# Kernel optimization log

Hardware: AMD Instinct MI355X
Metric: run time of the kernel (lower is better)

The kernel has to match this reference:

```python
import jax, jax.numpy as jnp
import numpy as np

B, T, D_IN, H, D_OUT = 4096, 512, 8, 50, 1

def setup_inputs() -> dict:
    key = jax.random.key(0)
    ks = jax.random.split(key, 7)
    s_ih = 1.0 / np.sqrt(H)
    return {
        "x": jax.random.normal(ks[0], (B, T, D_IN), dtype=jnp.float32),
        # torch nn.RNN params: weight_ih_l0 [H, D_IN], weight_hh_l0 [H, H], biases [H]
        "W_ih": jax.random.uniform(ks[1], (H, D_IN), minval=-s_ih, maxval=s_ih, dtype=jnp.float32),
        "W_hh": jax.random.uniform(ks[2], (H, H), minval=-s_ih, maxval=s_ih, dtype=jnp.float32),
        "b_ih": jax.random.uniform(ks[3], (H,), minval=-s_ih, maxval=s_ih, dtype=jnp.float32),
        "b_hh": jax.random.uniform(ks[4], (H,), minval=-s_ih, maxval=s_ih, dtype=jnp.float32),
        # fc: Linear(H, D_OUT)
        "fc_W": jax.random.uniform(ks[5], (D_OUT, H), minval=-s_ih, maxval=s_ih, dtype=jnp.float32),
        "fc_b": jax.random.uniform(ks[6], (D_OUT,), minval=-s_ih, maxval=s_ih, dtype=jnp.float32),
    }

def reference(x, W_ih, W_hh, b_ih, b_hh, fc_W, fc_b):
    # Vanilla RNN: h_t = tanh(x_t @ W_ih^T + b_ih + h_{t-1} @ W_hh^T + b_hh)
    # Precompute input projections for all timesteps (one big GEMM),
    # then scan the recurrence over time. Only the last hidden state is
    # needed because the module reads out[:, -1, :].
    xW = jnp.einsum('btd,hd->bth', x, W_ih) + (b_ih + b_hh)  # [B, T, H]
    xW_t = jnp.swapaxes(xW, 0, 1)  # [T, B, H] for scan over time

    def step(h, xw_t):
        h_new = jnp.tanh(xw_t + h @ W_hh.T)
        return h_new, None

    h0 = jnp.zeros((x.shape[0], W_hh.shape[0]), dtype=x.dtype)
    h_last, _ = jax.lax.scan(step, h0, xW_t)
    # fc on last timestep hidden
    return h_last @ fc_W.T + fc_b  # [B, D_OUT]
```

## Files before the change

### kernel.cpp

```cpp
#include <hip/hip_runtime.h>

#define B_TOT 4096
#define T_LEN 512
#define DIN   8
#define H_DIM 50

typedef __attribute__((ext_vector_type(8))) short  short8;
typedef __attribute__((ext_vector_type(4))) float  floatx4;

__device__ __forceinline__ ushort f2bf_rne(float f) {
  uint u = __float_as_uint(f);
  u += 0x7FFFu + ((u >> 16) & 1u);
  return (ushort)(u >> 16);
}
__device__ __forceinline__ ushort f2bf_trunc(float f) {
  return (ushort)(__float_as_uint(f) >> 16);
}
__device__ __forceinline__ float bf2f(ushort b) {
  return __uint_as_float(((uint)b) << 16);
}
__device__ __forceinline__ float fast_tanh(float v) {
  float e = __expf(2.0f * v);
  return 1.0f - 2.0f * __builtin_amdgcn_rcpf(1.0f + e);
}

#define ROWS 72
#define REG  1152

__global__ __launch_bounds__(256) void rnn_fused(
    const float* __restrict__ x, const float* __restrict__ W_ih,
    const float* __restrict__ W_hh, const float* __restrict__ b_ih,
    const float* __restrict__ b_hh, const float* __restrict__ fc_W,
    const float* __restrict__ fc_b, float* __restrict__ out)
{
  __shared__ __align__(16) ushort lds[4 * REG];

  const int tid  = threadIdx.x;
  const int lane = tid & 63;
  const int wave = tid >> 6;
  const int col  = lane & 15;
  const int kg   = lane >> 4;
  const int b0   = blockIdx.x * 16;

  const int iGlob = wave * 16 + col;
  union U8 { ushort u[8]; short8 v; };
  U8 Bh0u, Bh1u, Bl0u, Bl1u;
#pragma unroll
  for (int hf = 0; hf < 2; ++hf) {
#pragma unroll
    for (int j = 0; j < 8; ++j) {
      int k = hf * 32 + kg * 8 + j;
      float w = 0.f;
      if (iGlob < H_DIM) {
        if (k < H_DIM)            w = W_hh[iGlob * H_DIM + k];
        else if (k < H_DIM + DIN) w = W_ih[iGlob * DIN + (k - H_DIM)];
      }
      ushort hi = f2bf_rne(w);
      ushort lo = f2bf_trunc(w - bf2f(hi));
      if (hf == 0) { Bh0u.u[j] = hi; Bl0u.u[j] = lo; }
      else         { Bh1u.u[j] = hi; Bl1u.u[j] = lo; }
    }
  }
  const short8 Bh0 = Bh0u.v, Bh1 = Bh1u.v, Bl0 = Bl0u.v, Bl1 = Bl1u.v;

  const float bv = (iGlob < H_DIM) ? (b_ih[iGlob] + b_hh[iGlob]) : 0.f;
  const floatx4 biasf = {bv, bv, bv, bv};

  for (int z = tid; z < 4 * REG; z += 256) lds[z] = 0;
  __syncthreads();

  const int xm = tid >> 3;
  const int xd = tid & 7;
  const float* xp = x + ((size_t)(b0 + ((tid < 128) ? xm : 0)) * T_LEN) * DIN + xd;
  float px1 = 0.f, px2 = 0.f, px3 = 0.f;
  if (tid < 128) {
    float x0 = xp[0];
    ushort xh = f2bf_rne(x0);
    lds[0 * REG + xm * ROWS + H_DIM + xd] = xh;
    lds[1 * REG + xm * ROWS + H_DIM + xd] = f2bf_trunc(x0 - bf2f(xh));
    px1 = xp[8]; px2 = xp[16]; px3 = xp[24];
  }
  __syncthreads();

  auto step = [&](int t, int offph, int offpl, int offqh, int offql) {
    const int rb = col * ROWS + kg * 8;
    short8 Ah0 = *(const short8*)(lds + offph + rb);
    short8 Ah1 = *(const short8*)(lds + offph + rb + 32);
    short8 Al0 = *(const short8*)(lds + offpl + rb);
    short8 Al1 = *(const short8*)(lds + offpl + rb + 32);

    floatx4 acc = biasf;
    acc = __builtin_amdgcn_mfma_f32_16x16x32_bf16(Ah0, Bh0, acc, 0, 0, 0);
    acc = __builtin_amdgcn_mfma_f32_16x16x32_bf16(Ah1, Bh1, acc, 0, 0, 0);
    acc = __builtin_amdgcn_mfma_f32_16x16x32_bf16(Al0, Bh0, acc, 0, 0, 0);
    acc = __builtin_amdgcn_mfma_f32_16x16x32_bf16(Al1, Bh1, acc, 0, 0, 0);
    floatx4 accB = {0.f, 0.f, 0.f, 0.f};
    accB = __builtin_amdgcn_mfma_f32_16x16x32_bf16(Ah0, Bl0, accB, 0, 0, 0);
    accB = __builtin_amdgcn_mfma_f32_16x16x32_bf16(Ah1, Bl1, accB, 0, 0, 0);

    if (iGlob < H_DIM) {
#pragma unroll
      for (int r = 0; r < 4; ++r) {
        float v  = acc[r] + accB[r];
        float th = fast_tanh(v);
        ushort hi = f2bf_rne(th);
        ushort lo = f2bf_trunc(th - bf2f(hi));
        int m = kg * 4 + r;
        lds[offqh + m * ROWS + iGlob] = hi;
        lds[offql + m * ROWS + iGlob] = lo;
      }
    }
    if (tid < 128) {
      ushort xh = f2bf_rne(px1);
      ushort xl = f2bf_trunc(px1 - bf2f(xh));
      lds[offqh + xm * ROWS + H_DIM + xd] = xh;
      lds[offql + xm * ROWS + H_DIM + xd] = xl;
      px1 = px2; px2 = px3;
      int tn = t + 4; if (tn > T_LEN - 1) tn = T_LEN - 1;
      px3 = xp[tn * 8];
    }
    __syncthreads();
  };

  for (int t = 0; t < T_LEN; t += 2) {
    step(t,     0 * REG, 1 * REG, 2 * REG, 3 * REG);
    step(t + 1, 2 * REG, 3 * REG, 0 * REG, 1 * REG);
  }

  if (tid < 64) {
    int m = tid >> 2, kq = tid & 3;
    float acc2 = 0.f;
    for (int k = kq; k < H_DIM; k += 4) {
      float hv = bf2f(lds[0 * REG + m * ROWS + k]) + bf2f(lds[1 * REG + m * ROWS + k]);
      acc2 += hv * fc_W[k];
    }
    acc2 += __shfl_xor(acc2, 1);
    acc2 += __shfl_xor(acc2, 2);
    if (kq == 0) out[b0 + m] = acc2 + fc_b[0];
  }
}

extern "C" void kernel_launch(void* const* d_in, const int* in_sizes, int n_in,
                              void* d_out, int out_size, void* d_ws, size_t ws_size,
                              hipStream_t stream) {
  const float* x    = (const float*)d_in[0];
  const float* W_ih = (const float*)d_in[1];
  const float* W_hh = (const float*)d_in[2];
  const float* b_ih = (const float*)d_in[3];
  const float* b_hh = (const float*)d_in[4];
  const float* fc_W = (const float*)d_in[5];
  const float* fc_b = (const float*)d_in[6];
  rnn_fused<<<dim3(B_TOT / 16), dim3(256), 0, stream>>>(
      x, W_ih, W_hh, b_ih, b_hh, fc_W, fc_b, (float*)d_out);
}
```

Baseline: 296.9 us.

## Replace split-bf16 MFMA recurrence with per-wave FP32 FMA and register-resident weights

The split-bf16 MFMA recurrence is replaced with plain FP32 FMAs. Each lane keeps four hidden units' worth of combined W_hh/W_ih weights (232 floats) in registers, and each wave owns four batch rows with its own double-buffered LDS state. This removes the block-wide __syncthreads per timestep, the hi/lo bf16 conversions and the MFMA chain latency. It also fuses the final fc into a cross-lane shuffle reduction. The cost is very high register pressure (launch bounds of 1 block, possible spills) and about 232 scalar FMAs per lane per step on the serial critical path.

```diff
diff --git a/kernel.cpp b/kernel.cpp
--- a/kernel.cpp
+++ b/kernel.cpp
@@ -4,140 +4,110 @@
 #define T_LEN 512
 #define DIN   8
 #define H_DIM 50
+#define KTOT  58
+#define ROWF  80
 
-typedef __attribute__((ext_vector_type(8))) short  short8;
-typedef __attribute__((ext_vector_type(4))) float  floatx4;
+typedef __attribute__((ext_vector_type(4))) float floatx4;
 
-__device__ __forceinline__ ushort f2bf_rne(float f) {
-  uint u = __float_as_uint(f);
-  u += 0x7FFFu + ((u >> 16) & 1u);
-  return (ushort)(u >> 16);
-}
-__device__ __forceinline__ ushort f2bf_trunc(float f) {
-  return (ushort)(__float_as_uint(f) >> 16);
-}
-__device__ __forceinline__ float bf2f(ushort b) {
-  return __uint_as_float(((uint)b) << 16);
-}
 __device__ __forceinline__ float fast_tanh(float v) {
   float e = __expf(2.0f * v);
   return 1.0f - 2.0f * __builtin_amdgcn_rcpf(1.0f + e);
 }
 
-#define ROWS 72
-#define REG  1152
-
-__global__ __launch_bounds__(256) void rnn_fused(
+__global__ __launch_bounds__(256, 1) void rnn_fused(
     const float* __restrict__ x, const float* __restrict__ W_ih,
     const float* __restrict__ W_hh, const float* __restrict__ b_ih,
     const float* __restrict__ b_hh, const float* __restrict__ fc_W,
     const float* __restrict__ fc_b, float* __restrict__ out)
 {
-  __shared__ __align__(16) ushort lds[4 * REG];
+  __shared__ __align__(16) float hb[4][2][4][ROWF];
 
   const int tid  = threadIdx.x;
+  const int wv   = tid >> 6;
   const int lane = tid & 63;
-  const int wave = tid >> 6;
-  const int col  = lane & 15;
-  const int kg   = lane >> 4;
-  const int b0   = blockIdx.x * 16;
+  const int m    = lane >> 4;
+  const int i    = lane & 15;
+  const int bb   = blockIdx.x * 16 + wv * 4 + m;
 
-  const int iGlob = wave * 16 + col;
-  union U8 { ushort u[8]; short8 v; };
-  U8 Bh0u, Bh1u, Bl0u, Bl1u;
+  float wreg[4][KTOT];
+  float bias[4], fcw[4];
 #pragma unroll
-  for (int hf = 0; hf < 2; ++hf) {
+  for (int a = 0; a < 4; ++a) {
+    const int n = a * 16 + i;
+    const bool live = (n < H_DIM);
 #pragma unroll
-    for (int j = 0; j < 8; ++j) {
-      int k = hf * 32 + kg * 8 + j;
-      float w = 0.f;
-      if (iGlob < H_DIM) {
-        if (k < H_DIM)            w = W_hh[iGlob * H_DIM + k];
-        else if (k < H_DIM + DIN) w = W_ih[iGlob * DIN + (k - H_DIM)];
-      }
-      ushort hi = f2bf_rne(w);
-      ushort lo = f2bf_trunc(w - bf2f(hi));
-      if (hf == 0) { Bh0u.u[j] = hi; Bl0u.u[j] = lo; }
-      else         { Bh1u.u[j] = hi; Bl1u.u[j] = lo; }
+    for (int k = 0; k < H_DIM; ++k)
+      wreg[a][k] = live ? W_hh[n * H_DIM + k] : 0.f;
+#pragma unroll
+    for (int d = 0; d < DIN; ++d)
+      wreg[a][H_DIM + d] = live ? W_ih[n * DIN + d] : 0.f;
+    bias[a] = live ? (b_ih[n] + b_hh[n]) : 0.f;
+    fcw[a]  = live ? fc_W[n] : 0.f;
+  }
+
+  {
+    float* zb = &hb[wv][0][0][0];
+    for (int z = lane; z < 2 * 4 * ROWF; z += 64) zb[z] = 0.f;
+  }
+
+  const int xm = lane >> 3;
+  const int xd = lane & 7;
+  const bool xthr = (lane < 32);
+  const float* xp = x +
+      ((size_t)(blockIdx.x * 16 + wv * 4 + (xthr ? xm : 0)) * T_LEN) * DIN + xd;
+  float px0 = 0.f, px1 = 0.f, px2 = 0.f;
+  if (xthr) {
+    hb[wv][0][xm][H_DIM + xd] = xp[0];
+    px0 = xp[DIN]; px1 = xp[2 * DIN]; px2 = xp[3 * DIN];
+  }
+
+  float th0 = 0.f, th1 = 0.f, th2 = 0.f, th3 = 0.f;
+
+  auto body = [&](int t, float* curb, float* nxtb) {
+    const float* hr = curb + m * ROWF;
+    floatx4 hv[15];
+#pragma unroll
+    for (int j = 0; j < 15; ++j) hv[j] = *(const floatx4*)(hr + 4 * j);
+
+    float a0 = bias[0], a1 = bias[1], a2 = bias[2], a3 = bias[3];
+#pragma unroll
+    for (int k = 0; k < KTOT; ++k) {
+      const float h = hv[k >> 2][k & 3];
+      a0 = fmaf(wreg[0][k], h, a0);
+      a1 = fmaf(wreg[1][k], h, a1);
+      a2 = fmaf(wreg[2][k], h, a2);
+      a3 = fmaf(wreg[3][k], h, a3);
     }
-  }
-  const short8 Bh0 = Bh0u.v, Bh1 = Bh1u.v, Bl0 = Bl0u.v, Bl1 = Bl1u.v;
+    th0 = fast_tanh(a0); th1 = fast_tanh(a1);
+    th2 = fast_tanh(a2); th3 = fast_tanh(a3);
 
-  const float bv = (iGlob < H_DIM) ? (b_ih[iGlob] + b_hh[iGlob]) : 0.f;
-  const floatx4 biasf = {bv, bv, bv, bv};
+    float* hw = nxtb + m * ROWF;
+    hw[i]      = th0;
+    hw[16 + i] = th1;
+    hw[32 + i] = th2;
+    if (i < 2) hw[48 + i] = th3;
 
-  for (int z = tid; z < 4 * REG; z += 256) lds[z] = 0;
-  __syncthreads();
-
-  const int xm = tid >> 3;
-  const int xd = tid & 7;
-  const float* xp = x + ((size_t)(b0 + ((tid < 128) ? xm : 0)) * T_LEN) * DIN + xd;
-  float px1 = 0.f, px2 = 0.f, px3 = 0.f;
-  if (tid < 128) {
-    float x0 = xp[0];
-    ushort xh = f2bf_rne(x0);
-    lds[0 * REG + xm * ROWS + H_DIM + xd] = xh;
-    lds[1 * REG + xm * ROWS + H_DIM + xd] = f2bf_trunc(x0 - bf2f(xh));
-    px1 = xp[8]; px2 = xp[16]; px3 = xp[24];
-  }
-  __syncthreads();
-
-  auto step = [&](int t, int offph, int offpl, int offqh, int offql) {
-    const int rb = col * ROWS + kg * 8;
-    short8 Ah0 = *(const short8*)(lds + offph + rb);
-    short8 Ah1 = *(const short8*)(lds + offph + rb + 32);
-    short8 Al0 = *(const short8*)(lds + offpl + rb);
-    short8 Al1 = *(const short8*)(lds + offpl + rb + 32);
-
-    floatx4 acc = biasf;
-    acc = __builtin_amdgcn_mfma_f32_16x16x32_bf16(Ah0, Bh0, acc, 0, 0, 0);
-    acc = __builtin_amdgcn_mfma_f32_16x16x32_bf16(Ah1, Bh1, acc, 0, 0, 0);
-    acc = __builtin_amdgcn_mfma_f32_16x16x32_bf16(Al0, Bh0, acc, 0, 0, 0);
-    acc = __builtin_amdgcn_mfma_f32_16x16x32_bf16(Al1, Bh1, acc, 0, 0, 0);
-    floatx4 accB = {0.f, 0.f, 0.f, 0.f};
-    accB = __builtin_amdgcn_mfma_f32_16x16x32_bf16(Ah0, Bl0, accB, 0, 0, 0);
-    accB = __builtin_amdgcn_mfma_f32_16x16x32_bf16(Ah1, Bl1, accB, 0, 0, 0);
-
-    if (iGlob < H_DIM) {
-#pragma unroll
-      for (int r = 0; r < 4; ++r) {
-        float v  = acc[r] + accB[r];
-        float th = fast_tanh(v);
-        ushort hi = f2bf_rne(th);
-        ushort lo = f2bf_trunc(th - bf2f(hi));
-        int m = kg * 4 + r;
-        lds[offqh + m * ROWS + iGlob] = hi;
-        lds[offql + m * ROWS + iGlob] = lo;
-      }
+    if (xthr) {
+      nxtb[xm * ROWF + H_DIM + xd] = px0;
+      px0 = px1; px1 = px2;
+      int tn = t + 4; if (tn > T_LEN - 1) tn = T_LEN - 1;
+      px2 = xp[(size_t)tn * DIN];
     }
-    if (tid < 128) {
-      ushort xh = f2bf_rne(px1);
-      ushort xl = f2bf_trunc(px1 - bf2f(xh));
-      lds[offqh + xm * ROWS + H_DIM + xd] = xh;
-      lds[offql + xm * ROWS + H_DIM + xd] = xl;
-      px1 = px2; px2 = px3;
-      int tn = t + 4; if (tn > T_LEN - 1) tn = T_LEN - 1;
-      px3 = xp[tn * 8];
-    }
-    __syncthreads();
   };
 
+  float* b0p = &hb[wv][0][0][0];
+  float* b1p = &hb[wv][1][0][0];
   for (int t = 0; t < T_LEN; t += 2) {
-    step(t,     0 * REG, 1 * REG, 2 * REG, 3 * REG);
-    step(t + 1, 2 * REG, 3 * REG, 0 * REG, 1 * REG);
+    body(t,     b0p, b1p);
+    body(t + 1, b1p, b0p);
   }
 
-  if (tid < 64) {
-    int m = tid >> 2, kq = tid & 3;
-    float acc2 = 0.f;
-    for (int k = kq; k < H_DIM; k += 4) {
-      float hv = bf2f(lds[0 * REG + m * ROWS + k]) + bf2f(lds[1 * REG + m * ROWS + k]);
-      acc2 += hv * fc_W[k];
-    }
-    acc2 += __shfl_xor(acc2, 1);
-    acc2 += __shfl_xor(acc2, 2);
-    if (kq == 0) out[b0 + m] = acc2 + fc_b[0];
-  }
+  float p = th0 * fcw[0] + th1 * fcw[1] + th2 * fcw[2] + th3 * fcw[3];
+  p += __shfl_xor(p, 1);
+  p += __shfl_xor(p, 2);
+  p += __shfl_xor(p, 4);
+  p += __shfl_xor(p, 8);
+  if (i == 0) out[bb] = p + fc_b[0];
 }
 
 extern "C" void kernel_launch(void* const* d_in, const int* in_sizes, int n_in,
```

New measurement: 611.1 us. 106% more time.
